# Kernel optimization log

Measured on AMD Instinct MI355X. Metric: run time of the kernel, lower is better.

Reference implementation:

```python
import jax, jax.numpy as jnp
import numpy as np

N = 100000        # nodes
E_RAND = 1500000  # random edges (plus N self-loops)
NFEAT = 64
NHID = 64
NHEADS = 8
ALPHA = 0.2       # leaky-relu slope


def setup_inputs() -> dict:
    key = jax.random.key(0)
    ks = jax.random.split(key, 10)
    x = jax.random.normal(ks[0], (N, NFEAT), jnp.float32)
    src = jax.random.randint(ks[1], (E_RAND,), 0, N)
    dst = jax.random.randint(ks[2], (E_RAND,), 0, N)
    loops = jnp.arange(N)
    edge_index = jnp.stack([jnp.concatenate([src, loops]),
                            jnp.concatenate([dst, loops])]).astype(jnp.int32)
    s = 0.1
    W_att = jax.random.normal(ks[3], (NHEADS, NFEAT, NHID), jnp.float32) * s
    a_att = jax.random.normal(ks[4], (NHEADS, 2 * NHID), jnp.float32) * s
    W_out = jax.random.normal(ks[5], (NHEADS * NHID, NFEAT), jnp.float32) * s
    a_out = jax.random.normal(ks[6], (2 * NFEAT,), jnp.float32) * s
    W1 = jax.random.normal(ks[7], (NFEAT, NFEAT * 10), jnp.float32) * s
    b1 = jnp.zeros((NFEAT * 10,), jnp.float32)
    W2 = jax.random.normal(ks[8], (NFEAT * 10, 10), jnp.float32) * s
    b2 = jnp.zeros((10,), jnp.float32)
    W3 = jax.random.normal(ks[9], (10, 1), jnp.float32) * s
    b3 = jnp.zeros((1,), jnp.float32)
    return dict(x=x, edge_index=edge_index, W_att=W_att, a_att=a_att,
                W_out=W_out, a_out=a_out, W1=W1, b1=b1, W2=W2, b2=b2,
                W3=W3, b3=b3)


def _gat_layer(x, row, col, W, a, concat):
    # x: [N,F], W: [F,D], a: [2D]. Faithful to pyGAT SpGraphAttentionLayer:
    # edge_e = exp(-leakyrelu(a . [h_src || h_dst])), normalized by rowsum.
    n = x.shape[0]
    h = x @ W                                   # [N, D]
    d = h.shape[1]
    alpha_src = h @ a[:d]                       # [N]
    alpha_dst = h @ a[d:]                       # [N]
    score = alpha_src[row] + alpha_dst[col]     # [E]
    edge_e = jnp.exp(-jax.nn.leaky_relu(score, ALPHA))   # [E]
    rowsum = jax.ops.segment_sum(edge_e, row, num_segments=n)            # [N]
    h_prime = jax.ops.segment_sum(edge_e[:, None] * h[col], row,
                                  num_segments=n)                        # [N, D]
    h_prime = h_prime / rowsum[:, None]
    return jax.nn.elu(h_prime) if concat else h_prime


def reference(x, edge_index, W_att, a_att, W_out, a_out, W1, b1, W2, b2, W3, b3):
    row, col = edge_index[0], edge_index[1]
    # multi-head attention, concat along features
    heads = jax.vmap(lambda W, a: _gat_layer(x, row, col, W, a, True))(W_att, a_att)  # [H,N,D]
    xh = jnp.transpose(heads, (1, 0, 2)).reshape(x.shape[0], -1)  # [N, H*D]
    xo = jax.nn.elu(_gat_layer(xh, row, col, W_out, a_out, False))  # [N, NFEAT]
    # dense MLP head
    z = jax.nn.relu(xo @ W1 + b1)
    z = jax.nn.relu(z @ W2 + b2)
    z = jax.nn.sigmoid(z @ W3 + b3)  # [N, 1]
    return z
```

## Files before the change

kernel.cpp:

```cpp
#include <hip/hip_runtime.h>
#include <hip/hip_bf16.h>
#include <math.h>

#define NF 64
#define NH 8
#define SLOPE 0.2f

typedef __hip_bfloat16 bf16;
typedef short short8 __attribute__((ext_vector_type(8)));
typedef unsigned int uint4v __attribute__((ext_vector_type(4)));
typedef float f32x4 __attribute__((ext_vector_type(4)));
typedef float f32x2 __attribute__((ext_vector_type(2)));

__device__ __forceinline__ float us2f(unsigned short u){
  union{ unsigned int i; float f; } c; c.i = ((unsigned int)u) << 16; return c.f;
}
__device__ __forceinline__ float lo16(unsigned int u){
  union{ unsigned int i; float f; } c; c.i = u << 16; return c.f;
}
__device__ __forceinline__ float hi16(unsigned int u){
  union{ unsigned int i; float f; } c; c.i = u & 0xFFFF0000u; return c.f;
}
__device__ __forceinline__ unsigned short f2b_rne(float v){
  union{ float f; unsigned int i; } c; c.f = v;
  unsigned int b = c.i + 0x7FFF + ((c.i >> 16) & 1);
  return (unsigned short)(b >> 16);
}
__device__ __forceinline__ f32x4 mfma16(short8 a, short8 b, f32x4 c){
  return __builtin_amdgcn_mfma_f32_16x16x32_bf16(a, b, c, 0, 0, 0);
}


__global__ void k_prep1(const float* __restrict__ Watt, const float* __restrict__ aatt,
                        short* __restrict__ Bp1){
  int f = blockIdx.x >> 1, ks = blockIdx.x & 1;
  int lane = threadIdx.x;
  int kg = lane >> 4, cl = lane & 15;
  int col = f * 16 + cl;
  for (int j = 0; j < 8; j++){
    int k = ks * 32 + kg * 8 + j;
    float val;
    if (col < 512){
      val = Watt[(size_t)(col >> 6) * 4096 + k * 64 + (col & 63)];
    } else {
      int h = (col - 512) & 7;
      const float* arow = aatt + h * 128 + ((col >= 520) ? 64 : 0);
      const float* wrow = Watt + (size_t)h * 4096 + k * 64;
      float s = 0.f;
      for (int d = 0; d < 64; d++) s += wrow[d] * arow[d];
      val = s;
    }
    unsigned short hu = f2b_rne(val);
    float lof = val - us2f(hu);
    Bp1[((size_t)(ks * 33) + f) * 512 + lane * 8 + j]       = (short)hu;
    Bp1[((size_t)((2 + ks) * 33) + f) * 512 + lane * 8 + j] = (short)f2b_rne(lof);
  }
}

__global__ void k_prep2(const float* __restrict__ Wout, const float* __restrict__ aout,
                        short* __restrict__ Bp2){
  int f = blockIdx.x >> 4, ks = blockIdx.x & 15;
  int lane = threadIdx.x;
  int kg = lane >> 4, cl = lane & 15;
  int col = f * 16 + cl;
  for (int j = 0; j < 8; j++){
    int k = ks * 32 + kg * 8 + j;
    float val = 0.f;
    if (col < 64){
      val = Wout[(size_t)k * 64 + col];
    } else if (col == 64 || col == 65){
      const float* arow = aout + ((col == 65) ? 64 : 0);
      const float* wrow = Wout + (size_t)k * 64;
      float s = 0.f;
      for (int d = 0; d < 64; d++) s += wrow[d] * arow[d];
      val = s;
    }
    unsigned short hu = f2b_rne(val);
    float lof = val - us2f(hu);
    Bp2[((size_t)(ks * 5) + f) * 512 + lane * 8 + j]        = (short)hu;
    Bp2[((size_t)((16 + ks) * 5) + f) * 512 + lane * 8 + j] = (short)f2b_rne(lof);
  }
}

__global__ void k_prep3(const float* __restrict__ W1, short* __restrict__ Bp3){
  int f = blockIdx.x >> 1, ks = blockIdx.x & 1;
  int lane = threadIdx.x;
  int kg = lane >> 4, cl = lane & 15;
  int col = f * 16 + cl;
  for (int j = 0; j < 8; j++){
    int k = ks * 32 + kg * 8 + j;
    float val = W1[(size_t)k * 640 + col];
    unsigned short hu = f2b_rne(val);
    float lof = val - us2f(hu);
    Bp3[((size_t)(ks * 40) + f) * 512 + lane * 8 + j]       = (short)hu;
    Bp3[((size_t)((2 + ks) * 40) + f) * 512 + lane * 8 + j] = (short)f2b_rne(lof);
  }
}

__global__ void k_prep4(const float* __restrict__ W2, short* __restrict__ Bp4){
  int ks = blockIdx.x;
  int lane = threadIdx.x;
  int kg = lane >> 4, cl = lane & 15;
  for (int j = 0; j < 8; j++){
    int k = ks * 32 + kg * 8 + j;
    float val = (cl < 10) ? W2[k * 10 + cl] : 0.f;
    unsigned short hu = f2b_rne(val);
    Bp4[((size_t)ks) * 512 + lane * 8 + j]        = (short)hu;
    Bp4[((size_t)(20 + ks)) * 512 + lane * 8 + j] = (short)f2b_rne(val - us2f(hu));
  }
}

__global__ void __launch_bounds__(256)
k_prep_x(const float* __restrict__ x, const short* __restrict__ Bp1,
         short* __restrict__ xb, float* __restrict__ a1s, float* __restrict__ a1d,
         int n_nodes){
  __shared__ short xsh[16][72];
  __shared__ short xsl[16][72];
  int n0 = blockIdx.x * 16;
  int t = threadIdx.x;
  for (int i = t; i < 16 * 64; i += 256){
    int r = i >> 6, c = i & 63;
    int nn = n0 + r;
    float v = (nn < n_nodes) ? x[(size_t)nn * NF + c] : 0.f;
    unsigned short hu = f2b_rne(v);
    float lof = v - us2f(hu);
    xsh[r][c] = (short)hu;
    xsl[r][c] = (short)f2b_rne(lof);
  }
  __syncthreads();
  for (int i = t; i < 16 * 8; i += 256){
    int r = i >> 3, c8 = (i & 7) * 8;
    int nn = n0 + r;
    if (nn < n_nodes)
      *reinterpret_cast<short8*>(xb + (size_t)nn * 64 + c8) =
        *reinterpret_cast<const short8*>(&xsh[r][c8]);
  }
  int wid = t >> 6, lane = t & 63;
  if (wid == 3){
    int rowa = lane & 15, kg = lane >> 4, cl = lane & 15;
    short8 ah[2], al[2];
    #pragma unroll
    for (int ks = 0; ks < 2; ks++){
      ah[ks] = *reinterpret_cast<const short8*>(&xsh[rowa][ks * 32 + kg * 8]);
      al[ks] = *reinterpret_cast<const short8*>(&xsl[rowa][ks * 32 + kg * 8]);
    }
    f32x4 acc = {0.f, 0.f, 0.f, 0.f};
    #pragma unroll
    for (int ks = 0; ks < 2; ks++){
      short8 b_h = *reinterpret_cast<const short8*>(Bp1 + ((size_t)(ks * 33) + 32) * 512 + lane * 8);
      short8 b_l = *reinterpret_cast<const short8*>(Bp1 + ((size_t)((2 + ks) * 33) + 32) * 512 + lane * 8);
      acc = mfma16(ah[ks], b_h, acc);
      acc = mfma16(al[ks], b_h, acc);
      acc = mfma16(ah[ks], b_l, acc);
    }
    #pragma unroll
    for (int reg = 0; reg < 4; reg++){
      int nn = n0 + kg * 4 + reg;
      if (nn < n_nodes){
        if (cl < 8) a1s[nn * NH + cl] = acc[reg];
        else        a1d[nn * NH + (cl - 8)] = acc[reg];
      }
    }
  }
}

__global__ void k_count(const int* __restrict__ row, int* __restrict__ cnt, int E){
  int e = blockIdx.x * blockDim.x + threadIdx.x;
  if (e < E) atomicAdd(&cnt[row[e]], 1);
}

__global__ void k_scan_a(const int* __restrict__ cnt, int* __restrict__ incl,
                         int* __restrict__ bsum, int n){
  __shared__ int s[1024];
  int i = blockIdx.x * 1024 + threadIdx.x;
  int v = (i < n) ? cnt[i] : 0;
  s[threadIdx.x] = v;
  __syncthreads();
  for (int d = 1; d < 1024; d <<= 1){
    int tv = (threadIdx.x >= d) ? s[threadIdx.x - d] : 0;
    __syncthreads();
    s[threadIdx.x] += tv;
    __syncthreads();
  }
  if (i < n) incl[i] = s[threadIdx.x];
  if (threadIdx.x == 1023) bsum[blockIdx.x] = s[1023];
}

__global__ void k_scan_b(const int* __restrict__ bsum, int* __restrict__ boff, int nb){
  __shared__ int s[128];
  int t = threadIdx.x;
  if (nb <= 128){
    int v = (t < nb) ? bsum[t] : 0;
    s[t] = v;
    __syncthreads();
    for (int d = 1; d < 128; d <<= 1){
      int tv = (t >= d) ? s[t - d] : 0;
      __syncthreads();
      s[t] += tv;
      __syncthreads();
    }
    if (t < nb) boff[t] = s[t] - v;
  } else if (t == 0){
    int run = 0;
    for (int b = 0; b < nb; b++){ boff[b] = run; run += bsum[b]; }
  }
}

__global__ void k_scan_c(const int* __restrict__ incl, const int* __restrict__ cnt,
                         const int* __restrict__ boff, int* __restrict__ rowptr,
                         int* __restrict__ wptr, int n){
  int i = blockIdx.x * 1024 + threadIdx.x;
  if (i < n){
    int start = incl[i] - cnt[i] + boff[blockIdx.x];
    rowptr[i] = start;
    wptr[i]   = start;
  }
}

__global__ void k_scatter(const int* __restrict__ row, const int* __restrict__ col,
                          int* __restrict__ wptr, int* __restrict__ scol, int E){
  int e = blockIdx.x * blockDim.x + threadIdx.x;
  if (e < E){
    int r = row[e];
    int pos = atomicAdd(&wptr[r], 1);
    scol[pos] = col[e];
  }
}

__global__ void __launch_bounds__(512, 2)
k_agg1_gemm2(const short* __restrict__ xb, const float* __restrict__ a1s,
             const float* __restrict__ a1d, const int* __restrict__ rowptr,
             const int* __restrict__ cnt, const int* __restrict__ scol,
             const short* __restrict__ Bp1, const short* __restrict__ Bp2,
             bf16* __restrict__ h2b, float* __restrict__ a2s,
             float* __restrict__ a2d, int n_nodes){
  __shared__ short Gh[8 * 600];
  __shared__ short xh[8][528];
  int n0   = blockIdx.x * 8;
  int wid  = threadIdx.x >> 6;
  int lane = threadIdx.x & 63;
  int kg = lane >> 4, cl = lane & 15;
  int hsel = lane & 7;
  int n = n0 + wid;

  if (n < n_nodes){
    int beg = rowptr[n], deg = cnt[n];
    float asrc = a1s[n * NH + hsel];
    f32x4 accD[4];
    #pragma unroll
    for (int fb = 0; fb < 4; fb++){ accD[fb][0]=0.f; accD[fb][1]=0.f; accD[fb][2]=0.f; accD[fb][3]=0.f; }
    float rsum_part = 0.f;
    for (int p = 0; p < deg; p += 32){
      int c[8];
      #pragma unroll
      for (int j = 0; j < 8; j++){
        int kk = p + kg * 8 + j;
        c[j] = scol[beg + ((kk < deg) ? kk : 0)];
      }
      float ef[8];
      #pragma unroll
      for (int j = 0; j < 8; j++){
        float s = asrc + a1d[c[j] * NH + hsel];
        float l = fmaxf(s, SLOPE * s);
        float e = __expf(-l);
        ef[j] = ((p + kg * 8 + j) < deg) ? e : 0.f;
        rsum_part += ef[j];
      }
      short8 bfrag;
      #pragma unroll
      for (int j = 0; j < 8; j++) bfrag[j] = (short)f2b_rne(ef[j]);
      #pragma unroll
      for (int fb = 0; fb < 4; fb++){
        short8 afrag;
        #pragma unroll
        for (int j = 0; j < 8; j++)
          afrag[j] = xb[c[j] * 64 + fb * 16 + cl];
        accD[fb] = mfma16(afrag, bfrag, accD[fb]);
      }
    }
    float rsum = rsum_part;
    rsum += __shfl_xor(rsum, 16);
    rsum += __shfl_xor(rsum, 32);
    float inv = 1.f / rsum;
    if (cl < 8){
      #pragma unroll
      for (int fb = 0; fb < 4; fb++){
        #pragma unroll
        for (int reg = 0; reg < 4; reg++)
          Gh[wid * 600 + cl * 72 + fb * 16 + kg * 4 + reg] =
            (short)f2b_rne(accD[fb][reg] * inv);
      }
    }
  } else {
    if (cl < 8){
      #pragma unroll
      for (int fb = 0; fb < 4; fb++){
        #pragma unroll
        for (int reg = 0; reg < 4; reg++)
          Gh[wid * 600 + cl * 72 + fb * 16 + kg * 4 + reg] = 0;
      }
    }
  }
  __syncthreads();

  {
    int rowa = lane & 7;
    short8 gah[2];
    #pragma unroll
    for (int ks = 0; ks < 2; ks++)
      gah[ks] = *reinterpret_cast<const short8*>(&Gh[rowa * 600 + wid * 72 + ks * 32 + kg * 8]);
    #pragma unroll
    for (int fc = 0; fc < 4; fc++){
      int f = wid * 4 + fc;
      f32x4 acc = {0.f, 0.f, 0.f, 0.f};
      #pragma unroll
      for (int ks = 0; ks < 2; ks++){
        short8 b_h = *reinterpret_cast<const short8*>(Bp1 + ((size_t)(ks * 33) + f) * 512 + lane * 8);
        short8 b_l = *reinterpret_cast<const short8*>(Bp1 + ((size_t)((2 + ks) * 33) + f) * 512 + lane * 8);
        acc = mfma16(gah[ks], b_h, acc);
        acc = mfma16(gah[ks], b_l, acc);
      }
      if (kg < 2){
        #pragma unroll
        for (int reg = 0; reg < 4; reg++){
          int r = kg * 4 + reg;
          float v = acc[reg];
          v = (v > 0.f) ? v : (__expf(v) - 1.f);
          xh[r][wid * 64 + fc * 16 + cl] = (short)f2b_rne(v);
        }
      }
    }
  }
  __syncthreads();

  if (wid < 5){
    int rowa = lane & 7;
    f32x4 acc = {0.f, 0.f, 0.f, 0.f};
    #pragma unroll 4
    for (int ks = 0; ks < 16; ks++){
      short8 a_h = *reinterpret_cast<const short8*>(&xh[rowa][ks * 32 + kg * 8]);
      short8 b_h = *reinterpret_cast<const short8*>(Bp2 + ((size_t)(ks * 5) + wid) * 512 + lane * 8);
      short8 b_l = *reinterpret_cast<const short8*>(Bp2 + ((size_t)((16 + ks) * 5) + wid) * 512 + lane * 8);
      acc = mfma16(a_h, b_h, acc);
      acc = mfma16(a_h, b_l, acc);
    }
    if (kg < 2){
      #pragma unroll
      for (int reg = 0; reg < 4; reg++){
        int nn = n0 + kg * 4 + reg;
        if (nn < n_nodes){
          if (wid < 4){
            h2b[(size_t)nn * 64 + wid * 16 + cl] = __float2bfloat16(acc[reg]);
          } else if (cl == 0){
            a2s[nn] = acc[reg];
          } else if (cl == 1){
            a2d[nn] = acc[reg];
          }
        }
      }
    }
  }
}

__global__ void __launch_bounds__(256)
k_agg2(const bf16* __restrict__ h2b, const float* __restrict__ a2s,
       const float* __restrict__ a2d, const int* __restrict__ rowptr,
       const int* __restrict__ cnt, const int* __restrict__ scol,
       float* __restrict__ xo, int n_nodes){
  int wid  = threadIdx.x >> 6;
  int lane = threadIdx.x & 63;
  int g = lane >> 3, sl = lane & 7;
  int n = blockIdx.x * 32 + wid * 8 + g;
  bool nv = (n < n_nodes);
  int beg = 0, deg = 0;
  float asrc = 0.f;
  if (nv){ beg = rowptr[n]; deg = cnt[n]; asrc = a2s[n]; }
  int mdeg = deg;
  #pragma unroll
  for (int m = 8; m < 64; m <<= 1){
    int o = __shfl_xor(mdeg, m);
    mdeg = (o > mdeg) ? o : mdeg;
  }
  f32x2 acc2[4] = {{0.f,0.f},{0.f,0.f},{0.f,0.f},{0.f,0.f}};
  float rsum = 0.f;
  int it = 0;
  for (; it + 1 < mdeg; it += 2){
    int i0 = (it     < deg) ? it     : 0;
    int i1 = (it + 1 < deg) ? it + 1 : 0;
    int c0 = scol[beg + i0];
    int c1 = scol[beg + i1];
    uint4v h0 = *reinterpret_cast<const uint4v*>(h2b + ((size_t)c0 << 6) + sl * 8);
    uint4v h1 = *reinterpret_cast<const uint4v*>(h2b + ((size_t)c1 << 6) + sl * 8);
    float s0 = asrc + a2d[c0];
    float s1 = asrc + a2d[c1];
    float l0 = fmaxf(s0, SLOPE * s0);
    float l1 = fmaxf(s1, SLOPE * s1);
    float e0 = __expf(-l0);
    float e1 = __expf(-l1);
    e0 = (it     < deg) ? e0 : 0.f;
    e1 = (it + 1 < deg) ? e1 : 0.f;
    rsum += e0 + e1;
    f32x2 ev0 = {e0, e0}, ev1 = {e1, e1};
    #pragma unroll
    for (int d = 0; d < 4; d++){
      f32x2 hv0 = {lo16(h0[d]), hi16(h0[d])};
      f32x2 hv1 = {lo16(h1[d]), hi16(h1[d])};
      acc2[d] += ev0 * hv0 + ev1 * hv1;
    }
  }
  if (it < mdeg){
    int i0 = (it < deg) ? it : 0;
    int c0 = scol[beg + i0];
    uint4v h0 = *reinterpret_cast<const uint4v*>(h2b + ((size_t)c0 << 6) + sl * 8);
    float s0 = asrc + a2d[c0];
    float l0 = fmaxf(s0, SLOPE * s0);
    float e0 = __expf(-l0);
    e0 = (it < deg) ? e0 : 0.f;
    rsum += e0;
    f32x2 ev0 = {e0, e0};
    #pragma unroll
    for (int d = 0; d < 4; d++){
      f32x2 hv0 = {lo16(h0[d]), hi16(h0[d])};
      acc2[d] += ev0 * hv0;
    }
  }
  if (nv){
    float inv = 1.f / rsum;
    float4 lo, hi;
    float vv[8];
    #pragma unroll
    for (int jj = 0; jj < 8; jj++){
      float v = acc2[jj >> 1][jj & 1] * inv;
      vv[jj] = (v > 0.f) ? v : (__expf(v) - 1.f);
    }
    lo.x = vv[0]; lo.y = vv[1]; lo.z = vv[2]; lo.w = vv[3];
    hi.x = vv[4]; hi.y = vv[5]; hi.z = vv[6]; hi.w = vv[7];
    *reinterpret_cast<float4*>(xo + (size_t)n * 64 + sl * 8)     = lo;
    *reinterpret_cast<float4*>(xo + (size_t)n * 64 + sl * 8 + 4) = hi;
  }
}

__global__ void __launch_bounds__(256)
k_mlp(const float* __restrict__ xo, const short* __restrict__ Bp3,
      const short* __restrict__ Bp4, const float* __restrict__ b1,
      const float* __restrict__ b2, const float* __restrict__ W3,
      const float* __restrict__ b3, float* __restrict__ out, int n_nodes){
  __shared__ short xsh[16][72];
  __shared__ short xsl[16][72];
  __shared__ short z1h[16][648];
  __shared__ float part[4][16][16];
  __shared__ float z2[16][10];
  int n0 = blockIdx.x * 16;
  int t  = threadIdx.x;
  for (int i = t; i < 16 * 64; i += 256){
    int r = i >> 6, c = i & 63;
    int nn = n0 + r;
    float v = (nn < n_nodes) ? xo[(size_t)nn * 64 + c] : 0.f;
    unsigned short hu = f2b_rne(v);
    float lof = v - us2f(hu);
    xsh[r][c] = (short)hu;
    xsl[r][c] = (short)f2b_rne(lof);
  }
  __syncthreads();
  int wid = t >> 6, lane = t & 63;
  int rowa = lane & 15, kg = lane >> 4, cl = lane & 15;
  {
    short8 ah[2], al[2];
    #pragma unroll
    for (int ks = 0; ks < 2; ks++){
      ah[ks] = *reinterpret_cast<const short8*>(&xsh[rowa][ks * 32 + kg * 8]);
      al[ks] = *reinterpret_cast<const short8*>(&xsl[rowa][ks * 32 + kg * 8]);
    }
    for (int f0 = 0; f0 < 10; f0++){
      int f = wid * 10 + f0;
      f32x4 acc = {0.f, 0.f, 0.f, 0.f};
      #pragma unroll
      for (int ks = 0; ks < 2; ks++){
        short8 b_h = *reinterpret_cast<const short8*>(Bp3 + ((size_t)(ks * 40) + f) * 512 + lane * 8);
        short8 b_l = *reinterpret_cast<const short8*>(Bp3 + ((size_t)((2 + ks) * 40) + f) * 512 + lane * 8);
        acc = mfma16(ah[ks], b_h, acc);
        acc = mfma16(al[ks], b_h, acc);
        acc = mfma16(ah[ks], b_l, acc);
      }
      int cc = f * 16 + cl;
      float bb = b1[cc];
      #pragma unroll
      for (int reg = 0; reg < 4; reg++)
        z1h[kg * 4 + reg][cc] = (short)f2b_rne(fmaxf(acc[reg] + bb, 0.f));
    }
  }
  __syncthreads();
  {
    f32x4 acc = {0.f, 0.f, 0.f, 0.f};
    #pragma unroll
    for (int kk = 0; kk < 5; kk++){
      int ks = wid * 5 + kk;
      short8 a_h = *reinterpret_cast<const short8*>(&z1h[rowa][ks * 32 + kg * 8]);
      short8 b_h = *reinterpret_cast<const short8*>(Bp4 + ((size_t)ks) * 512 + lane * 8);
      short8 b_l = *reinterpret_cast<const short8*>(Bp4 + ((size_t)(20 + ks)) * 512 + lane * 8);
      acc = mfma16(a_h, b_h, acc);
      acc = mfma16(a_h, b_l, acc);
    }
    #pragma unroll
    for (int reg = 0; reg < 4; reg++)
      part[wid][kg * 4 + reg][cl] = acc[reg];
  }
  __syncthreads();
  if (t < 160){
    int r = t / 10, c = t % 10;
    float v = (part[0][r][c] + part[1][r][c]) + (part[2][r][c] + part[3][r][c]);
    z2[r][c] = fmaxf(v + b2[c], 0.f);
  }
  __syncthreads();
  if (t < 16){
    int nn = n0 + t;
    if (nn < n_nodes){
      float acc = b3[0];
      #pragma unroll
      for (int kk = 0; kk < 10; kk++) acc += z2[t][kk] * W3[kk];
      out[nn] = 1.f / (1.f + __expf(-acc));
    }
  }
}

extern "C" void kernel_launch(void* const* d_in, const int* in_sizes, int n_in,
                              void* d_out, int out_size, void* d_ws, size_t ws_size,
                              hipStream_t stream){
  const float* x    = (const float*)d_in[0];
  const int*   ei   = (const int*)  d_in[1];
  const float* Watt = (const float*)d_in[2];
  const float* aatt = (const float*)d_in[3];
  const float* Wout = (const float*)d_in[4];
  const float* aout = (const float*)d_in[5];
  const float* W1   = (const float*)d_in[6];
  const float* b1   = (const float*)d_in[7];
  const float* W2   = (const float*)d_in[8];
  const float* b2   = (const float*)d_in[9];
  const float* W3   = (const float*)d_in[10];
  const float* b3   = (const float*)d_in[11];
  float* out = (float*)d_out;

  int N = in_sizes[0] / NF;
  int E = in_sizes[1] / 2;
  const int* row = ei;
  const int* col = ei + E;

  char* base = (char*)d_ws;
  size_t off = 0;
  auto alloc = [&](size_t bytes) -> void* {
    void* p = base + off;
    off = (off + bytes + 255) & ~(size_t)255;
    return p;
  };
  short* xb     = (short*)alloc((size_t)N * 64 * 2);
  bf16*  h2b    = (bf16*) alloc((size_t)N * 64 * 2);
  float* xo     = (float*)alloc((size_t)N * 64 * 4);
  float* a1s    = (float*)alloc((size_t)N * NH * 4);
  float* a1d    = (float*)alloc((size_t)N * NH * 4);
  float* a2s    = (float*)alloc((size_t)N * 4);
  float* a2d    = (float*)alloc((size_t)N * 4);
  int*   cnt    = (int*)  alloc((size_t)N * 4);
  int*   rowptr = (int*)  alloc((size_t)N * 4);
  int*   wptr   = (int*)  alloc((size_t)N * 4);
  int*   incl   = (int*)  alloc((size_t)N * 4);
  int    NB     = (N + 1023) / 1024;
  int*   bsum   = (int*)  alloc((size_t)NB * 4);
  int*   boff   = (int*)  alloc((size_t)NB * 4);
  int*   scol   = (int*)  alloc((size_t)E * 4);
  short* Bp1    = (short*)alloc((size_t)4 * 33 * 512 * 2);
  short* Bp2    = (short*)alloc((size_t)32 * 5 * 512 * 2);
  short* Bp3    = (short*)alloc((size_t)4 * 40 * 512 * 2);
  short* Bp4    = (short*)alloc((size_t)40 * 512 * 2);
  (void)ws_size; (void)n_in; (void)out_size;

  hipMemsetAsync(cnt, 0, (size_t)N * 4, stream);

  k_prep1     <<<66,              64, 0, stream>>>(Watt, aatt, Bp1);
  k_prep2     <<<80,              64, 0, stream>>>(Wout, aout, Bp2);
  k_prep3     <<<80,              64, 0, stream>>>(W1, Bp3);
  k_prep4     <<<20,              64, 0, stream>>>(W2, Bp4);
  k_prep_x    <<<(N + 15) / 16,  256, 0, stream>>>(x, Bp1, xb, a1s, a1d, N);
  k_count     <<<(E + 255) / 256, 256, 0, stream>>>(row, cnt, E);
  k_scan_a    <<<NB,             1024, 0, stream>>>(cnt, incl, bsum, N);
  k_scan_b    <<<1,               128, 0, stream>>>(bsum, boff, NB);
  k_scan_c    <<<NB,             1024, 0, stream>>>(incl, cnt, boff, rowptr, wptr, N);
  k_scatter   <<<(E + 255) / 256, 256, 0, stream>>>(row, col, wptr, scol, E);
  k_agg1_gemm2<<<(N + 7) / 8,     512, 0, stream>>>(xb, a1s, a1d, rowptr, cnt, scol,
                                                    Bp1, Bp2, h2b, a2s, a2d, N);
  k_agg2      <<<(N + 31) / 32,  256, 0, stream>>>(h2b, a2s, a2d, rowptr, cnt, scol, xo, N);
  k_mlp       <<<(N + 15) / 16,  256, 0, stream>>>(xo, Bp3, Bp4, b1, b2, W3, b3, out, N);
}
```

Measured before the change: 522.6 us.

## Compute second-layer aggregation with MFMA, one wavefront per node

Rewrites k_agg2 so each wavefront processes a single destination node. It gathers neighbor rows 32 edges at a time and accumulates the attention-weighted sum with bf16 16x16x32 MFMA instructions instead of per-lane packed FMAs. It also drops the per-group max-degree loop, which made every 8-lane group wait for the highest-degree node in its wave. In exchange, neighbor features are now loaded as scalar 16-bit gathers instead of 128-bit vector loads, the edge weights are rounded to bf16, and with an average degree of about 16 roughly half of each 32-edge MFMA tile is padding.

```diff
diff --git a/kernel.cpp b/kernel.cpp
--- a/kernel.cpp
+++ b/kernel.cpp
@@ -14,12 +14,6 @@
 
 __device__ __forceinline__ float us2f(unsigned short u){
   union{ unsigned int i; float f; } c; c.i = ((unsigned int)u) << 16; return c.f;
-}
-__device__ __forceinline__ float lo16(unsigned int u){
-  union{ unsigned int i; float f; } c; c.i = u << 16; return c.f;
-}
-__device__ __forceinline__ float hi16(unsigned int u){
-  union{ unsigned int i; float f; } c; c.i = u & 0xFFFF0000u; return c.f;
 }
 __device__ __forceinline__ unsigned short f2b_rne(float v){
   union{ float f; unsigned int i; } c; c.f = v;
@@ -367,76 +361,58 @@
        const float* __restrict__ a2d, const int* __restrict__ rowptr,
        const int* __restrict__ cnt, const int* __restrict__ scol,
        float* __restrict__ xo, int n_nodes){
+  const short* h2s = reinterpret_cast<const short*>(h2b);
   int wid  = threadIdx.x >> 6;
   int lane = threadIdx.x & 63;
-  int g = lane >> 3, sl = lane & 7;
-  int n = blockIdx.x * 32 + wid * 8 + g;
-  bool nv = (n < n_nodes);
-  int beg = 0, deg = 0;
-  float asrc = 0.f;
-  if (nv){ beg = rowptr[n]; deg = cnt[n]; asrc = a2s[n]; }
-  int mdeg = deg;
+  int kg = lane >> 4, cl = lane & 15;
+  int n = blockIdx.x * 4 + wid;
+  if (n >= n_nodes) return;
+  float asrc = a2s[n];
+  int beg = rowptr[n], deg = cnt[n];
+  f32x4 accD[4];
   #pragma unroll
-  for (int m = 8; m < 64; m <<= 1){
-    int o = __shfl_xor(mdeg, m);
-    mdeg = (o > mdeg) ? o : mdeg;
-  }
-  f32x2 acc2[4] = {{0.f,0.f},{0.f,0.f},{0.f,0.f},{0.f,0.f}};
-  float rsum = 0.f;
-  int it = 0;
-  for (; it + 1 < mdeg; it += 2){
-    int i0 = (it     < deg) ? it     : 0;
-    int i1 = (it + 1 < deg) ? it + 1 : 0;
-    int c0 = scol[beg + i0];
-    int c1 = scol[beg + i1];
-    uint4v h0 = *reinterpret_cast<const uint4v*>(h2b + ((size_t)c0 << 6) + sl * 8);
-    uint4v h1 = *reinterpret_cast<const uint4v*>(h2b + ((size_t)c1 << 6) + sl * 8);
-    float s0 = asrc + a2d[c0];
-    float s1 = asrc + a2d[c1];
-    float l0 = fmaxf(s0, SLOPE * s0);
-    float l1 = fmaxf(s1, SLOPE * s1);
-    float e0 = __expf(-l0);
-    float e1 = __expf(-l1);
-    e0 = (it     < deg) ? e0 : 0.f;
-    e1 = (it + 1 < deg) ? e1 : 0.f;
-    rsum += e0 + e1;
-    f32x2 ev0 = {e0, e0}, ev1 = {e1, e1};
-    #pragma unroll
-    for (int d = 0; d < 4; d++){
-      f32x2 hv0 = {lo16(h0[d]), hi16(h0[d])};
-      f32x2 hv1 = {lo16(h1[d]), hi16(h1[d])};
-      acc2[d] += ev0 * hv0 + ev1 * hv1;
-    }
-  }
-  if (it < mdeg){
-    int i0 = (it < deg) ? it : 0;
-    int c0 = scol[beg + i0];
-    uint4v h0 = *reinterpret_cast<const uint4v*>(h2b + ((size_t)c0 << 6) + sl * 8);
-    float s0 = asrc + a2d[c0];
-    float l0 = fmaxf(s0, SLOPE * s0);
-    float e0 = __expf(-l0);
-    e0 = (it < deg) ? e0 : 0.f;
-    rsum += e0;
-    f32x2 ev0 = {e0, e0};
-    #pragma unroll
-    for (int d = 0; d < 4; d++){
-      f32x2 hv0 = {lo16(h0[d]), hi16(h0[d])};
-      acc2[d] += ev0 * hv0;
-    }
-  }
-  if (nv){
-    float inv = 1.f / rsum;
-    float4 lo, hi;
-    float vv[8];
-    #pragma unroll
-    for (int jj = 0; jj < 8; jj++){
-      float v = acc2[jj >> 1][jj & 1] * inv;
-      vv[jj] = (v > 0.f) ? v : (__expf(v) - 1.f);
-    }
-    lo.x = vv[0]; lo.y = vv[1]; lo.z = vv[2]; lo.w = vv[3];
-    hi.x = vv[4]; hi.y = vv[5]; hi.z = vv[6]; hi.w = vv[7];
-    *reinterpret_cast<float4*>(xo + (size_t)n * 64 + sl * 8)     = lo;
-    *reinterpret_cast<float4*>(xo + (size_t)n * 64 + sl * 8 + 4) = hi;
+  for (int fb = 0; fb < 4; fb++){ accD[fb][0]=0.f; accD[fb][1]=0.f; accD[fb][2]=0.f; accD[fb][3]=0.f; }
+  float rsum_part = 0.f;
+  for (int p = 0; p < deg; p += 32){
+    int c[8];
+    #pragma unroll
+    for (int j = 0; j < 8; j++){
+      int kk = p + kg * 8 + j;
+      c[j] = scol[beg + ((kk < deg) ? kk : 0)];
+    }
+    float ef[8];
+    #pragma unroll
+    for (int j = 0; j < 8; j++){
+      float s = asrc + a2d[c[j]];
+      float l = fmaxf(s, SLOPE * s);
+      float e = __expf(-l);
+      ef[j] = ((p + kg * 8 + j) < deg) ? e : 0.f;
+      rsum_part += ef[j];
+    }
+    short8 bfrag;
+    #pragma unroll
+    for (int j = 0; j < 8; j++) bfrag[j] = (short)f2b_rne(ef[j]);
+    #pragma unroll
+    for (int fb = 0; fb < 4; fb++){
+      short8 afrag;
+      #pragma unroll
+      for (int j = 0; j < 8; j++)
+        afrag[j] = h2s[c[j] * 64 + fb * 16 + cl];
+      accD[fb] = mfma16(afrag, bfrag, accD[fb]);
+    }
+  }
+  float rsum = rsum_part;
+  rsum += __shfl_xor(rsum, 16);
+  rsum += __shfl_xor(rsum, 32);
+  float inv = 1.f / rsum;
+  if (cl < 4){
+    f32x4 sel = (cl == 0) ? accD[0] : (cl == 1) ? accD[1] : (cl == 2) ? accD[2] : accD[3];
+    float4 v;
+    float u0 = sel[0] * inv; v.x = (u0 > 0.f) ? u0 : (__expf(u0) - 1.f);
+    float u1 = sel[1] * inv; v.y = (u1 > 0.f) ? u1 : (__expf(u1) - 1.f);
+    float u2 = sel[2] * inv; v.z = (u2 > 0.f) ? u2 : (__expf(u2) - 1.f);
+    float u3 = sel[3] * inv; v.w = (u3 > 0.f) ? u3 : (__expf(u3) - 1.f);
+    *reinterpret_cast<float4*>(xo + (size_t)n * 64 + cl * 16 + kg * 4) = v;
   }
 }
 
@@ -587,6 +563,6 @@
   k_scatter   <<<(E + 255) / 256, 256, 0, stream>>>(row, col, wptr, scol, E);
   k_agg1_gemm2<<<(N + 7) / 8,     512, 0, stream>>>(xb, a1s, a1d, rowptr, cnt, scol,
                                                     Bp1, Bp2, h2b, a2s, a2d, N);
-  k_agg2      <<<(N + 31) / 32,  256, 0, stream>>>(h2b, a2s, a2d, rowptr, cnt, scol, xo, N);
+  k_agg2      <<<(N + 3) / 4,     256, 0, stream>>>(h2b, a2s, a2d, rowptr, cnt, scol, xo, N);
   k_mlp       <<<(N + 15) / 16,  256, 0, stream>>>(xo, Bp3, Bp4, b1, b2, W3, b3, out, N);
 }
```

Measured after the change: 543.2 us. 3.9% more time.
